# Optimization experiments

Hardware: AMD Instinct MI355X
Metric: run time of the kernel (lower is better)

Reference implementation:

```python
import jax, jax.numpy as jnp
import numpy as np

B, CF, HH, WW = 32, 768, 28, 28
M, NH = 32, 1024
BETA = 0.05

def _lin(key, out_d, in_d):
    k1, k2 = jax.random.split(key)
    s = 1.0 / np.sqrt(in_d)
    W = jax.random.uniform(k1, (out_d, in_d), minval=-s, maxval=s, dtype=jnp.float32)
    b = jax.random.uniform(k2, (out_d,), minval=-s, maxval=s, dtype=jnp.float32)
    return W, b

def setup_inputs() -> dict:
    key = jax.random.key(0)
    ks = jax.random.split(key, 16)
    inp = {
        'F': jax.random.normal(ks[0], (B, CF, HH, WW), dtype=jnp.float32),
        'A': jax.random.uniform(ks[1], (B, M, HH, WW), dtype=jnp.float32),
        'C': jax.random.normal(ks[2], (1, M * CF), dtype=jnp.float32),
    }
    names = ['xi', 'hi', 'xf', 'hf', 'xo', 'ho', 'xc', 'hc']
    for i, n in enumerate(names):
        in_d = CF if n[0] == 'x' else NH
        W, b = _lin(ks[3 + i], NH, in_d)
        inp['W' + n] = W
        inp['b' + n] = b
    return inp

def reference(F, A, C, Wxi, bxi, Whi, bhi, Wxf, bxf, Whf, bhf, Wxo, bxo, Who, bho, Wxc, bxc, Whc, bhc):
    b = F.shape[0]
    hw = F.shape[2] * F.shape[3]
    m = A.shape[1]
    # BAP: avg-pool of F * A_i over spatial dims, for each attention map -> [B, M, Cf]
    V = jnp.einsum('bchw,bmhw->bmc', F, A) / hw
    V = V.reshape(b, -1)  # [B, M*Cf]
    # RCLoss (center update + detached MSE)
    tmp = jnp.sum(V - C, axis=0)  # [M*Cf]
    C_new = C + (BETA * tmp / b)[None, :]
    diff = jax.lax.stop_gradient(V) - jax.lax.stop_gradient(C_new)
    rcloss = jnp.mean(diff * diff)
    # LSTM over M steps (note: original uses sigmoid for all gates via Sig_i)
    X_seq = V.reshape(b, m, -1).transpose(1, 0, 2)  # [M, B, Cf]
    h0 = jnp.zeros((b, Whi.shape[0]), dtype=V.dtype)
    c0 = jnp.zeros((b, Whi.shape[0]), dtype=V.dtype)
    def step(carry, X):
        H, Cc = carry
        I = jax.nn.sigmoid(X @ Wxi.T + bxi + H @ Whi.T + bhi)
        Fg = jax.nn.sigmoid(X @ Wxf.T + bxf + H @ Whf.T + bhf)
        O = jax.nn.sigmoid(X @ Wxo.T + bxo + H @ Who.T + bho)
        Ct = jnp.tanh(X @ Wxc.T + bxc + H @ Whc.T + bhc)
        Cc = Fg * Cc + I * Ct
        H = O * jnp.tanh(Cc)
        return (H, Cc), None
    (H, _), _ = jax.lax.scan(step, (h0, c0), X_seq)
    return (H, rcloss, C_new)
```

## Files before the change

kernel.cpp:

```cpp
#include <hip/hip_runtime.h>
#include <math.h>

#define CF 768
#define MM 32
#define HW 784
#define MCF 24576
#define BETA 0.05f

typedef __attribute__((ext_vector_type(8))) short bf16x8;
typedef __attribute__((ext_vector_type(4))) float f32x4;

__device__ __forceinline__ unsigned short bf16rne(float x) {
    unsigned int bits = __float_as_uint(x);
    unsigned int r = (bits + 0x7fffu + ((bits >> 16) & 1u)) >> 16;
    return (unsigned short)r;
}
__device__ __forceinline__ float bf2f(unsigned short u) {
    return __uint_as_float(((unsigned int)u) << 16);
}
__device__ __forceinline__ float sigf(float x) { return 1.f / (1.f + __expf(-x)); }
__device__ __forceinline__ float ftanh(float x) {
    x = fminf(fmaxf(x, -12.f), 12.f);
    float e = __expf(2.f * x);
    return (e - 1.f) / (e + 1.f);
}

__device__ __forceinline__ void cvt8(const float4 a, const float4 b, unsigned short* u) {
    u[0] = bf16rne(a.x); u[1] = bf16rne(a.y); u[2] = bf16rne(a.z); u[3] = bf16rne(a.w);
    u[4] = bf16rne(b.x); u[5] = bf16rne(b.y); u[6] = bf16rne(b.z); u[7] = bf16rne(b.w);
}

__global__ __launch_bounds__(256) void kA3(const float* __restrict__ F,
                                           const float* __restrict__ Ain,
                                           unsigned short* __restrict__ Vbf) {
    __shared__ unsigned short Alds[3328 * 8];
    __shared__ unsigned short Flds[2][512 * 8];
    const int bid = blockIdx.x;
    const int b = bid / 12, ct = bid - b * 12;
    const int cbase = ct * 64;
    const int t = threadIdx.x;
    const int lane = t & 63, w = t >> 6;
    const int n = lane & 15, q = lane >> 4;

    {
        float4 va[7][2];
        #pragma unroll
        for (int it = 0; it < 7; ++it) {
            int s = it * 256 + t;
            int lf = s & 63, mk = s >> 6;
            int m = (mk & 1) * 16 + (lf & 15);
            int k = (mk >> 1) * 32 + (lf >> 4) * 8;
            if (k < 784) {
                const float* src = Ain + ((size_t)(b * 32 + m)) * 784 + k;
                va[it][0] = *(const float4*)src;
                va[it][1] = *(const float4*)(src + 4);
            } else {
                va[it][0] = (float4){0, 0, 0, 0};
                va[it][1] = (float4){0, 0, 0, 0};
            }
        }
        #pragma unroll
        for (int it = 0; it < 7; ++it) {
            int s = it * 256 + t;
            unsigned short u[8];
            cvt8(va[it][0], va[it][1], u);
            *(uint4*)&Alds[s * 8] = *(const uint4*)u;
        }
        float4 vb[6][2];
        #pragma unroll
        for (int it = 0; it < 6; ++it) {
            int s = (it + 7) * 256 + t;
            int lf = s & 63, mk = s >> 6;
            int m = (mk & 1) * 16 + (lf & 15);
            int k = (mk >> 1) * 32 + (lf >> 4) * 8;
            if (k < 784) {
                const float* src = Ain + ((size_t)(b * 32 + m)) * 784 + k;
                vb[it][0] = *(const float4*)src;
                vb[it][1] = *(const float4*)(src + 4);
            } else {
                vb[it][0] = (float4){0, 0, 0, 0};
                vb[it][1] = (float4){0, 0, 0, 0};
            }
        }
        #pragma unroll
        for (int it = 0; it < 6; ++it) {
            int s = (it + 7) * 256 + t;
            unsigned short u[8];
            cvt8(vb[it][0], vb[it][1], u);
            *(uint4*)&Alds[s * 8] = *(const uint4*)u;
        }
    }

    float4 pf[2][2];
    const int s0 = t, s1 = t + 256;
    const int ls0 = s0 & 63, kc20 = (s0 >> 6) & 1, nt0 = s0 >> 7;
    const int ls1 = s1 & 63, kc21 = (s1 >> 6) & 1, nt1 = s1 >> 7;
    const int fc0 = nt0 * 16 + (ls0 & 15), fk0 = kc20 * 32 + (ls0 >> 4) * 8;
    const int fc1 = nt1 * 16 + (ls1 & 15), fk1 = kc21 * 32 + (ls1 >> 4) * 8;
    const float* Fr0 = F + ((size_t)(b * 768) + cbase + fc0) * 784;
    const float* Fr1 = F + ((size_t)(b * 768) + cbase + fc1) * 784;
    pf[0][0] = *(const float4*)(Fr0 + fk0); pf[0][1] = *(const float4*)(Fr0 + fk0 + 4);
    pf[1][0] = *(const float4*)(Fr1 + fk1); pf[1][1] = *(const float4*)(Fr1 + fk1 + 4);
    {
        unsigned short u[8];
        cvt8(pf[0][0], pf[0][1], u); *(uint4*)&Flds[0][s0 * 8] = *(const uint4*)u;
        cvt8(pf[1][0], pf[1][1], u); *(uint4*)&Flds[0][s1 * 8] = *(const uint4*)u;
    }
    __syncthreads();

    f32x4 acc[2];
    acc[0] = (f32x4){0, 0, 0, 0};
    acc[1] = (f32x4){0, 0, 0, 0};

    for (int c13 = 0; c13 < 13; ++c13) {
        const int buf = c13 & 1;
        if (c13 < 12) {
            int k0 = (c13 + 1) * 64 + fk0;
            int k1 = (c13 + 1) * 64 + fk1;
            if (k0 < 784) {
                pf[0][0] = *(const float4*)(Fr0 + k0); pf[0][1] = *(const float4*)(Fr0 + k0 + 4);
            } else { pf[0][0] = (float4){0,0,0,0}; pf[0][1] = (float4){0,0,0,0}; }
            if (k1 < 784) {
                pf[1][0] = *(const float4*)(Fr1 + k1); pf[1][1] = *(const float4*)(Fr1 + k1 + 4);
            } else { pf[1][0] = (float4){0,0,0,0}; pf[1][1] = (float4){0,0,0,0}; }
        }
        #pragma unroll
        for (int kc2 = 0; kc2 < 2; ++kc2) {
            const int kc = c13 * 2 + kc2;
            bf16x8 bfr = *(const bf16x8*)&Flds[buf][((w * 2 + kc2) * 64 + lane) * 8];
            bf16x8 a0 = *(const bf16x8*)&Alds[((kc * 2 + 0) * 64 + lane) * 8];
            bf16x8 a1 = *(const bf16x8*)&Alds[((kc * 2 + 1) * 64 + lane) * 8];
            acc[0] = __builtin_amdgcn_mfma_f32_16x16x32_bf16(a0, bfr, acc[0], 0, 0, 0);
            acc[1] = __builtin_amdgcn_mfma_f32_16x16x32_bf16(a1, bfr, acc[1], 0, 0, 0);
        }
        if (c13 < 12) {
            unsigned short u[8];
            cvt8(pf[0][0], pf[0][1], u); *(uint4*)&Flds[buf ^ 1][s0 * 8] = *(const uint4*)u;
            cvt8(pf[1][0], pf[1][1], u); *(uint4*)&Flds[buf ^ 1][s1 * 8] = *(const uint4*)u;
        }
        __syncthreads();
    }

    #pragma unroll
    for (int mt = 0; mt < 2; ++mt)
        #pragma unroll
        for (int r = 0; r < 4; ++r)
            Vbf[(size_t)(b * 32 + mt * 16 + q * 4 + r) * 768 + cbase + w * 16 + n] =
                bf16rne(acc[mt][r] * (1.f / 784.f));
}

__global__ __launch_bounds__(256) void kMisc(
    const unsigned short* __restrict__ Vbf, const float* __restrict__ C,
    float* __restrict__ Cnew_out, float* __restrict__ partial,
    const float* __restrict__ Wxi, const float* __restrict__ Wxf,
    const float* __restrict__ Wxo, const float* __restrict__ Wxc,
    unsigned short* __restrict__ Wxbf,
    const float* __restrict__ Whi, const float* __restrict__ Whf,
    const float* __restrict__ Who, const float* __restrict__ Whc,
    unsigned short* __restrict__ Wbf) {
    const int bid = blockIdx.x;
    if (bid < 96) {
        int j = bid * 256 + threadIdx.x;
        float c = C[j];
        float s = 0.f;
        for (int b = 0; b < 32; ++b) s += bf2f(Vbf[(size_t)b * MCF + j]);
        float cn = c + BETA * (s * (1.f / 32.f) - c);
        Cnew_out[j] = cn;
        float ds = 0.f;
        for (int b = 0; b < 32; ++b) {
            float d = bf2f(Vbf[(size_t)b * MCF + j]) - cn;
            ds = fmaf(d, d, ds);
        }
        __shared__ float red[256];
        red[threadIdx.x] = ds;
        __syncthreads();
        for (int off = 128; off > 0; off >>= 1) {
            if (threadIdx.x < off) red[threadIdx.x] += red[threadIdx.x + off];
            __syncthreads();
        }
        if (threadIdx.x == 0) partial[bid] = red[0];
    } else if (bid < 1632) {
        int gid = (bid - 96) * 256 + threadIdx.x;
        int row = gid / 96;
        int kq = (gid - row * 96) * 8;
        int g = row >> 10, j = row & 1023;
        const float* Wg = (g == 0) ? Wxi : (g == 1) ? Wxf : (g == 2) ? Wxo : Wxc;
        const float* src = Wg + (size_t)j * CF + kq;
        float4 f0 = *(const float4*)src;
        float4 f1 = *(const float4*)(src + 4);
        unsigned short u[8];
        cvt8(f0, f1, u);
        *(uint4*)&Wxbf[(size_t)row * CF + kq] = *(const uint4*)u;
    } else {
        size_t tid8 = ((size_t)(bid - 1632) * 256 + threadIdx.x) * 8;
        int row = (int)(tid8 >> 10);
        int k = (int)(tid8 & 1023);
        int g = row >> 10, j = row & 1023;
        const float* Wg = (g == 0) ? Whi : (g == 1) ? Whf : (g == 2) ? Who : Whc;
        const float* src = Wg + (size_t)j * 1024 + k;
        float4 f0 = *(const float4*)src;
        float4 f1 = *(const float4*)(src + 4);
        unsigned short u[8];
        cvt8(f0, f1, u);
        *(uint4*)&Wbf[tid8] = *(const uint4*)u;
    }
}

__global__ __launch_bounds__(512) void kC3(
    const unsigned short* __restrict__ Vbf,
    const unsigned short* __restrict__ Wxbf,
    const float* __restrict__ bxi, const float* __restrict__ bxf,
    const float* __restrict__ bxo, const float* __restrict__ bxc,
    const float* __restrict__ bhi, const float* __restrict__ bhf,
    const float* __restrict__ bho, const float* __restrict__ bhc,
    unsigned short* __restrict__ Xbf,
    const float* __restrict__ partial, float* __restrict__ outRC) {
    __shared__ unsigned short Asg[512 * 8];
    const int bx = blockIdx.x;
    const int by = blockIdx.y;
    const int t = threadIdx.x;
    const int lane = t & 63;
    const int w = t >> 6;
    const int n = lane & 15;
    const int q = lane >> 4;
    const int mbase = bx * 64;

    const int st_row = (w & 3) * 16 + n;
    const int st_kb  = (w >> 2) * 4 + q;
    const int st_rg  = mbase + st_row;
    const int st_vrow = (st_rg & 31) * 32 + (st_rg >> 5);
    const unsigned short* st_src = Vbf + (size_t)st_vrow * CF + st_kb * 8;

    const int nb = by * 128 + w * 16;
    const unsigned short* Brow = Wxbf + (size_t)(nb + n) * CF + q * 8;

    f32x4 acc[4];
    #pragma unroll
    for (int g = 0; g < 4; ++g) acc[g] = (f32x4){0.f, 0.f, 0.f, 0.f};

    uint4 st = *(const uint4*)st_src;
    for (int kc = 0; kc < 12; ++kc) {
        __syncthreads();
        *(uint4*)&Asg[t * 8] = st;
        __syncthreads();
        if (kc + 1 < 12) st = *(const uint4*)(st_src + (kc + 1) * 64);
        #pragma unroll
        for (int p = 0; p < 2; ++p) {
            bf16x8 bfr = *(const bf16x8*)(Brow + kc * 64 + p * 32);
            #pragma unroll
            for (int g = 0; g < 4; ++g) {
                bf16x8 a = *(const bf16x8*)&Asg[((p * 4 + g) * 64 + lane) * 8];
                acc[g] = __builtin_amdgcn_mfma_f32_16x16x32_bf16(a, bfr, acc[g], 0, 0, 0);
            }
        }
    }

    const int gg = by >> 3;
    const int j = (by & 7) * 128 + w * 16 + n;
    const float* bx_ = (gg == 0) ? bxi : (gg == 1) ? bxf : (gg == 2) ? bxo : bxc;
    const float* bh_ = (gg == 0) ? bhi : (gg == 1) ? bhf : (gg == 2) ? bho : bhc;
    const float bias = bx_[j] + bh_[j];
    #pragma unroll
    for (int g = 0; g < 4; ++g) {
        #pragma unroll
        for (int rr = 0; rr < 4; ++rr) {
            int rg = mbase + g * 16 + q * 4 + rr;
            int tt = rg >> 5, bb = rg & 31;
            Xbf[((size_t)(tt * 4 + gg) * 32 + bb) * 1024 + j] = bf16rne(acc[g][rr] + bias);
        }
    }

    if (bx == 0 && by == 31) {
        __syncthreads();
        float* red = (float*)Asg;
        float v = (t < 96) ? partial[t] : 0.f;
        red[t] = v;
        __syncthreads();
        for (int off = 256; off > 0; off >>= 1) {
            if (t < off) red[t] += red[t + off];
            __syncthreads();
        }
        if (t == 0) outRC[0] = red[0] / (32.f * 24576.f);
    }
}

__global__ __launch_bounds__(512) void kStep(
    const unsigned short* __restrict__ Wbf,
    const unsigned short* __restrict__ Xbf,
    const unsigned short* __restrict__ Hprev,
    unsigned short* __restrict__ Hnext,
    float* __restrict__ Cst,
    float* __restrict__ outH,
    int step) {
    __shared__ float pbuf[8][32][17];
    __shared__ float sbuf[32][17];
    const int bi = blockIdx.x;
    const int jbase = bi * 4;
    const int t = threadIdx.x;
    const int lane = t & 63;
    const int w = t >> 6;
    const int n = lane & 15;
    const int q = lane >> 4;

    const int pb = t >> 4, pnn = t & 15;
    const int pg = pnn >> 2, pjj = pnn & 3;
    const float xv = bf2f(Xbf[(((size_t)step * 4 + pg) * 32 + pb) * 1024 + jbase + pjj]);
    float cprev = 0.f;
    if (step > 0 && t < 128) cprev = Cst[(t >> 2) * 1024 + jbase + (t & 3)];

    if (step > 0) {
        const int g = n >> 2, jj = n & 3;
        const unsigned short* Wrow = Wbf + ((size_t)(g * 1024 + jbase + jj)) * 1024 + w * 128;
        const unsigned short* hb0 = Hprev + (size_t)n * 1024 + w * 128;
        const unsigned short* hb1 = Hprev + (size_t)(n + 16) * 1024 + w * 128;
        f32x4 acc0 = {0.f, 0.f, 0.f, 0.f};
        f32x4 acc1 = {0.f, 0.f, 0.f, 0.f};
        #pragma unroll
        for (int ks = 0; ks < 4; ++ks) {
            int k = ks * 32 + q * 8;
            bf16x8 bfrag = *(const bf16x8*)(Wrow + k);
            bf16x8 a0 = *(const bf16x8*)(hb0 + k);
            bf16x8 a1 = *(const bf16x8*)(hb1 + k);
            acc0 = __builtin_amdgcn_mfma_f32_16x16x32_bf16(a0, bfrag, acc0, 0, 0, 0);
            acc1 = __builtin_amdgcn_mfma_f32_16x16x32_bf16(a1, bfrag, acc1, 0, 0, 0);
        }
        #pragma unroll
        for (int r = 0; r < 4; ++r) {
            pbuf[w][q * 4 + r][n] = acc0[r];
            pbuf[w][16 + q * 4 + r][n] = acc1[r];
        }
    }
    __syncthreads();
    {
        float s = xv;
        if (step > 0) {
            #pragma unroll
            for (int w2 = 0; w2 < 8; ++w2) s += pbuf[w2][pb][pnn];
        }
        sbuf[pb][pnn] = s;
    }
    __syncthreads();
    if (t < 128) {
        int b = t >> 2, jj = t & 3;
        float I  = sigf(sbuf[b][jj]);
        float Fg = sigf(sbuf[b][4 + jj]);
        float O  = sigf(sbuf[b][8 + jj]);
        float Ct = ftanh(sbuf[b][12 + jj]);
        float c = fmaf(Fg, cprev, I * Ct);
        Cst[b * 1024 + jbase + jj] = c;
        float h = O * ftanh(c);
        if (step < 31) {
            Hnext[b * 1024 + jbase + jj] = bf16rne(h);
        } else {
            outH[b * 1024 + jbase + jj] = h;
        }
    }
}

extern "C" void kernel_launch(void* const* d_in, const int* in_sizes, int n_in,
                              void* d_out, int out_size, void* d_ws, size_t ws_size,
                              hipStream_t stream) {
    const float* F   = (const float*)d_in[0];
    const float* A   = (const float*)d_in[1];
    const float* C   = (const float*)d_in[2];
    const float* Wxi = (const float*)d_in[3];
    const float* bxi = (const float*)d_in[4];
    const float* Whi = (const float*)d_in[5];
    const float* bhi = (const float*)d_in[6];
    const float* Wxf = (const float*)d_in[7];
    const float* bxf = (const float*)d_in[8];
    const float* Whf = (const float*)d_in[9];
    const float* bhf = (const float*)d_in[10];
    const float* Wxo = (const float*)d_in[11];
    const float* bxo = (const float*)d_in[12];
    const float* Who = (const float*)d_in[13];
    const float* bho = (const float*)d_in[14];
    const float* Wxc = (const float*)d_in[15];
    const float* bxc = (const float*)d_in[16];
    const float* Whc = (const float*)d_in[17];
    const float* bhc = (const float*)d_in[18];

    float* out   = (float*)d_out;
    float* outH  = out;
    float* outRC = out + 32768;
    float* outC  = out + 32769;

    float* ws = (float*)d_ws;
    unsigned short* Xbf  = (unsigned short*)ws;
    unsigned short* Wxbf = (unsigned short*)(ws + 2097152);
    unsigned short* Wbf  = (unsigned short*)(ws + 3670016);
    unsigned short* Vbf  = (unsigned short*)(ws + 5767168);
    float* part = ws + 6160384;
    unsigned short* Hbf = (unsigned short*)(ws + 6160480);
    float* Cst  = ws + 6193248;

    kA3<<<dim3(384), 256, 0, stream>>>(F, A, Vbf);
    kMisc<<<dim3(3680), 256, 0, stream>>>(Vbf, C, outC, part,
                                          Wxi, Wxf, Wxo, Wxc, Wxbf,
                                          Whi, Whf, Who, Whc, Wbf);
    kC3<<<dim3(16, 32), 512, 0, stream>>>(Vbf, Wxbf,
                                          bxi, bxf, bxo, bxc,
                                          bhi, bhf, bho, bhc, Xbf,
                                          part, outRC);

    for (int step = 0; step < 32; ++step) {
        const unsigned short* Hprev = Hbf + ((step + 1) & 1) * 32768;
        unsigned short* Hnext = (unsigned short*)(Hbf + (step & 1) * 32768);
        kStep<<<dim3(256), 512, 0, stream>>>(Wbf, Xbf, Hprev, Hnext, Cst, outH, step);
    }
}
```

Before: 228.3 us.

## Fuse 32 LSTM step launches into one persistent kernel with atomic step barriers

Replaces the per-timestep kernel loop with a single persistent kernel of 128 blocks. Each block owns 8 hidden units, keeps the cell state in registers, and waits on per-step atomic counters (grouped by block index mod 8) before reading the previous hidden state. The previous hidden state is staged in shared memory per half of K, and the new hidden state is written to a rotating per-step buffer. This removes 31 kernel-launch boundaries and the global cell-state round trip, at the cost of spin-waiting and relying on all 128 blocks being co-resident.

```diff
diff --git a/kernel.cpp b/kernel.cpp
--- a/kernel.cpp
+++ b/kernel.cpp
@@ -284,75 +284,121 @@
     }
 }
 
-__global__ __launch_bounds__(512) void kStep(
+__global__ __launch_bounds__(1024) void kLP(
     const unsigned short* __restrict__ Wbf,
     const unsigned short* __restrict__ Xbf,
-    const unsigned short* __restrict__ Hprev,
-    unsigned short* __restrict__ Hnext,
-    float* __restrict__ Cst,
-    float* __restrict__ outH,
-    int step) {
-    __shared__ float pbuf[8][32][17];
-    __shared__ float sbuf[32][17];
+    unsigned short* __restrict__ Hrot,
+    unsigned int* __restrict__ cnt,
+    float* __restrict__ outH) {
+    __shared__ char smem[65536];
+    unsigned short* Hs = (unsigned short*)smem;
+    float* pb = (float*)(smem + 32768);
+    float* sb = (float*)smem;
     const int bi = blockIdx.x;
-    const int jbase = bi * 4;
+    const int jbase = bi * 8;
     const int t = threadIdx.x;
     const int lane = t & 63;
     const int w = t >> 6;
-    const int n = lane & 15;
-    const int q = lane >> 4;
-
-    const int pb = t >> 4, pnn = t & 15;
-    const int pg = pnn >> 2, pjj = pnn & 3;
-    const float xv = bf2f(Xbf[(((size_t)step * 4 + pg) * 32 + pb) * 1024 + jbase + pjj]);
-    float cprev = 0.f;
-    if (step > 0 && t < 128) cprev = Cst[(t >> 2) * 1024 + jbase + (t & 3)];
-
-    if (step > 0) {
-        const int g = n >> 2, jj = n & 3;
-        const unsigned short* Wrow = Wbf + ((size_t)(g * 1024 + jbase + jj)) * 1024 + w * 128;
-        const unsigned short* hb0 = Hprev + (size_t)n * 1024 + w * 128;
-        const unsigned short* hb1 = Hprev + (size_t)(n + 16) * 1024 + w * 128;
+    const int nh = w & 1, kw = w >> 1;
+    const int n16 = lane & 15, q = lane >> 4;
+
+    const int rown = nh * 16 + n16;
+    const int gB = rown >> 3, jjB = rown & 7;
+    const unsigned short* Wrow = Wbf + ((size_t)(gB * 1024 + jbase + jjB)) * 1024;
+
+    const int cb = t >> 2, cjp = t & 3;
+    float creg0 = 0.f, creg1 = 0.f;
+
+    for (int step = 0; step < 32; ++step) {
+        unsigned int xv0 = 0, xv1 = 0, xv2 = 0, xv3 = 0;
+        if (t < 128) {
+            xv0 = *(const unsigned int*)&Xbf[(((size_t)step * 4 + 0) * 32 + cb) * 1024 + jbase + cjp * 2];
+            xv1 = *(const unsigned int*)&Xbf[(((size_t)step * 4 + 1) * 32 + cb) * 1024 + jbase + cjp * 2];
+            xv2 = *(const unsigned int*)&Xbf[(((size_t)step * 4 + 2) * 32 + cb) * 1024 + jbase + cjp * 2];
+            xv3 = *(const unsigned int*)&Xbf[(((size_t)step * 4 + 3) * 32 + cb) * 1024 + jbase + cjp * 2];
+        }
+        if (step > 0 && t < 8) {
+            while (atomicAdd(&cnt[(step - 1) * 8 + t], 0u) < 16u)
+                __builtin_amdgcn_s_sleep(8);
+        }
+        __syncthreads();
+
         f32x4 acc0 = {0.f, 0.f, 0.f, 0.f};
         f32x4 acc1 = {0.f, 0.f, 0.f, 0.f};
-        #pragma unroll
-        for (int ks = 0; ks < 4; ++ks) {
-            int k = ks * 32 + q * 8;
-            bf16x8 bfrag = *(const bf16x8*)(Wrow + k);
-            bf16x8 a0 = *(const bf16x8*)(hb0 + k);
-            bf16x8 a1 = *(const bf16x8*)(hb1 + k);
-            acc0 = __builtin_amdgcn_mfma_f32_16x16x32_bf16(a0, bfrag, acc0, 0, 0, 0);
-            acc1 = __builtin_amdgcn_mfma_f32_16x16x32_bf16(a1, bfrag, acc1, 0, 0, 0);
-        }
-        #pragma unroll
-        for (int r = 0; r < 4; ++r) {
-            pbuf[w][q * 4 + r][n] = acc0[r];
-            pbuf[w][16 + q * 4 + r][n] = acc1[r];
-        }
-    }
-    __syncthreads();
-    {
-        float s = xv;
         if (step > 0) {
+            const unsigned short* Hprev = Hrot + (size_t)(step - 1) * 32768;
             #pragma unroll
-            for (int w2 = 0; w2 < 8; ++w2) s += pbuf[w2][pb][pnn];
-        }
-        sbuf[pb][pnn] = s;
-    }
-    __syncthreads();
-    if (t < 128) {
-        int b = t >> 2, jj = t & 3;
-        float I  = sigf(sbuf[b][jj]);
-        float Fg = sigf(sbuf[b][4 + jj]);
-        float O  = sigf(sbuf[b][8 + jj]);
-        float Ct = ftanh(sbuf[b][12 + jj]);
-        float c = fmaf(Fg, cprev, I * Ct);
-        Cst[b * 1024 + jbase + jj] = c;
-        float h = O * ftanh(c);
+            for (int half = 0; half < 2; ++half) {
+                #pragma unroll
+                for (int ss = 0; ss < 2; ++ss) {
+                    int s = t + ss * 1024;
+                    int ls = s & 63, grp = s >> 6;
+                    int mt_ = grp & 1, kc_ = grp >> 1;
+                    int m = mt_ * 16 + (ls & 15);
+                    int kk = kc_ * 32 + (ls >> 4) * 8;
+                    uint4 d = *(const uint4*)(Hprev + (size_t)m * 1024 + half * 512 + kk);
+                    *(uint4*)&Hs[(size_t)s * 8] = d;
+                }
+                __syncthreads();
+                #pragma unroll
+                for (int kc2 = 0; kc2 < 2; ++kc2) {
+                    int kcl = kw * 2 + kc2;
+                    bf16x8 bfr = *(const bf16x8*)(Wrow + half * 512 + kcl * 32 + q * 8);
+                    bf16x8 a0 = *(const bf16x8*)&Hs[((kcl * 2 + 0) * 64 + lane) * 8];
+                    bf16x8 a1 = *(const bf16x8*)&Hs[((kcl * 2 + 1) * 64 + lane) * 8];
+                    acc0 = __builtin_amdgcn_mfma_f32_16x16x32_bf16(a0, bfr, acc0, 0, 0, 0);
+                    acc1 = __builtin_amdgcn_mfma_f32_16x16x32_bf16(a1, bfr, acc1, 0, 0, 0);
+                }
+                __syncthreads();
+            }
+            #pragma unroll
+            for (int r = 0; r < 4; ++r) {
+                pb[((kw * 2 + nh) * 2 + 0) * 256 + (q * 4 + r) * 16 + n16] = acc0[r];
+                pb[((kw * 2 + nh) * 2 + 1) * 256 + (q * 4 + r) * 16 + n16] = acc1[r];
+            }
+        }
+        __syncthreads();
+        {
+            int b = t >> 5, r = t & 31;
+            float s = 0.f;
+            if (step > 0) {
+                int mt_ = b >> 4, m16 = b & 15, nh_ = r >> 4, nn = r & 15;
+                #pragma unroll
+                for (int k8 = 0; k8 < 8; ++k8)
+                    s += pb[((k8 * 2 + nh_) * 2 + mt_) * 256 + m16 * 16 + nn];
+            }
+            sb[r * 33 + b] = s;
+        }
+        __syncthreads();
+        if (t < 128) {
+            float p0 = bf2f((unsigned short)(xv0 & 0xffff)) + sb[(0 * 8 + cjp * 2) * 33 + cb];
+            float p1 = bf2f((unsigned short)(xv1 & 0xffff)) + sb[(1 * 8 + cjp * 2) * 33 + cb];
+            float p2 = bf2f((unsigned short)(xv2 & 0xffff)) + sb[(2 * 8 + cjp * 2) * 33 + cb];
+            float p3 = bf2f((unsigned short)(xv3 & 0xffff)) + sb[(3 * 8 + cjp * 2) * 33 + cb];
+            float I0 = sigf(p0), F0 = sigf(p1), O0 = sigf(p2), T0 = ftanh(p3);
+            creg0 = fmaf(F0, creg0, I0 * T0);
+            float h0 = O0 * ftanh(creg0);
+            float q0 = bf2f((unsigned short)(xv0 >> 16)) + sb[(0 * 8 + cjp * 2 + 1) * 33 + cb];
+            float q1 = bf2f((unsigned short)(xv1 >> 16)) + sb[(1 * 8 + cjp * 2 + 1) * 33 + cb];
+            float q2 = bf2f((unsigned short)(xv2 >> 16)) + sb[(2 * 8 + cjp * 2 + 1) * 33 + cb];
+            float q3 = bf2f((unsigned short)(xv3 >> 16)) + sb[(3 * 8 + cjp * 2 + 1) * 33 + cb];
+            float I1 = sigf(q0), F1 = sigf(q1), O1 = sigf(q2), T1 = ftanh(q3);
+            creg1 = fmaf(F1, creg1, I1 * T1);
+            float h1 = O1 * ftanh(creg1);
+
+            if (step < 31) {
+                unsigned int packed = (unsigned int)bf16rne(h0) | ((unsigned int)bf16rne(h1) << 16);
+                unsigned int* dst = (unsigned int*)(Hrot + (size_t)step * 32768);
+                atomicExch(dst + (cb * 512 + (jbase >> 1) + cjp), packed);
+            } else {
+                float2 hv; hv.x = h0; hv.y = h1;
+                *(float2*)&outH[cb * 1024 + jbase + cjp * 2] = hv;
+            }
+        }
         if (step < 31) {
-            Hnext[b * 1024 + jbase + jj] = bf16rne(h);
-        } else {
-            outH[b * 1024 + jbase + jj] = h;
+            asm volatile("s_waitcnt vmcnt(0)" ::: "memory");
+            __syncthreads();
+            if (t == 0) atomicAdd(&cnt[step * 8 + (bi & 7)], 1u);
         }
     }
 }
@@ -391,9 +437,10 @@
     unsigned short* Wbf  = (unsigned short*)(ws + 3670016);
     unsigned short* Vbf  = (unsigned short*)(ws + 5767168);
     float* part = ws + 6160384;
-    unsigned short* Hbf = (unsigned short*)(ws + 6160480);
-    float* Cst  = ws + 6193248;
-
+    unsigned short* Hrot = (unsigned short*)(ws + 6160480);
+    unsigned int* cnt = (unsigned int*)(ws + 6684768);
+
+    hipMemsetAsync(cnt, 0, 256 * sizeof(unsigned int), stream);
     kA3<<<dim3(384), 256, 0, stream>>>(F, A, Vbf);
     kMisc<<<dim3(3680), 256, 0, stream>>>(Vbf, C, outC, part,
                                           Wxi, Wxf, Wxo, Wxc, Wxbf,
@@ -402,10 +449,5 @@
                                           bxi, bxf, bxo, bxc,
                                           bhi, bhf, bho, bhc, Xbf,
                                           part, outRC);
-
-    for (int step = 0; step < 32; ++step) {
-        const unsigned short* Hprev = Hbf + ((step + 1) & 1) * 32768;
-        unsigned short* Hnext = (unsigned short*)(Hbf + (step & 1) * 32768);
-        kStep<<<dim3(256), 512, 0, stream>>>(Wbf, Xbf, Hprev, Hnext, Cst, outH, step);
-    }
-}
+    kLP<<<dim3(128), 1024, 0, stream>>>(Wbf, Xbf, Hrot, cnt, outH);
+}
```

New measurement: 278.7 us. 22.1% more time.

## Fold weight conversion into BAP kernel and RC-loss into input-GEMM kernel

Applied to the files above, without the earlier changes.

Removes the separate kMisc launch. The fp32→bf16 weight conversion blocks now run as extra blocks of the BAP kernel, so they overlap with the MFMA work. The center-update and RC-loss reduction run as extra blocks of the input-projection GEMM kernel and accumulate into the output with atomicAdd. This saves one launch and one serialization point. The cost is a float atomic accumulation order, which makes the loss sum order nondeterministic, and a mixed-workload grid in the first kernel.

```diff
diff --git a/kernel.cpp b/kernel.cpp
--- a/kernel.cpp
+++ b/kernel.cpp
@@ -30,15 +30,53 @@
     u[4] = bf16rne(b.x); u[5] = bf16rne(b.y); u[6] = bf16rne(b.z); u[7] = bf16rne(b.w);
 }
 
-__global__ __launch_bounds__(256) void kA3(const float* __restrict__ F,
-                                           const float* __restrict__ Ain,
-                                           unsigned short* __restrict__ Vbf) {
+__global__ __launch_bounds__(256) void kA3M(
+    const float* __restrict__ F, const float* __restrict__ Ain,
+    unsigned short* __restrict__ Vbf,
+    const float* __restrict__ Wxi, const float* __restrict__ Wxf,
+    const float* __restrict__ Wxo, const float* __restrict__ Wxc,
+    unsigned short* __restrict__ Wxbf,
+    const float* __restrict__ Whi, const float* __restrict__ Whf,
+    const float* __restrict__ Who, const float* __restrict__ Whc,
+    unsigned short* __restrict__ Wbf,
+    float* __restrict__ outRC) {
     __shared__ unsigned short Alds[3328 * 8];
     __shared__ unsigned short Flds[2][512 * 8];
     const int bid = blockIdx.x;
+    const int t = threadIdx.x;
+
+    if (bid >= 384) {
+        if (bid == 384 && t == 0) outRC[0] = 0.f;
+        if (bid < 1920) {
+            int gid = (bid - 384) * 256 + t;
+            int row = gid / 96;
+            int kq = (gid - row * 96) * 8;
+            int g = row >> 10, j = row & 1023;
+            const float* Wg = (g == 0) ? Wxi : (g == 1) ? Wxf : (g == 2) ? Wxo : Wxc;
+            const float* src = Wg + (size_t)j * CF + kq;
+            float4 f0 = *(const float4*)src;
+            float4 f1 = *(const float4*)(src + 4);
+            unsigned short u[8];
+            cvt8(f0, f1, u);
+            *(uint4*)&Wxbf[(size_t)row * CF + kq] = *(const uint4*)u;
+        } else {
+            size_t tid8 = ((size_t)(bid - 1920) * 256 + t) * 8;
+            int row = (int)(tid8 >> 10);
+            int k = (int)(tid8 & 1023);
+            int g = row >> 10, j = row & 1023;
+            const float* Wg = (g == 0) ? Whi : (g == 1) ? Whf : (g == 2) ? Who : Whc;
+            const float* src = Wg + (size_t)j * 1024 + k;
+            float4 f0 = *(const float4*)src;
+            float4 f1 = *(const float4*)(src + 4);
+            unsigned short u[8];
+            cvt8(f0, f1, u);
+            *(uint4*)&Wbf[tid8] = *(const uint4*)u;
+        }
+        return;
+    }
+
     const int b = bid / 12, ct = bid - b * 12;
     const int cbase = ct * 64;
-    const int t = threadIdx.x;
     const int lane = t & 63, w = t >> 6;
     const int n = lane & 15, q = lane >> 4;
 
@@ -149,64 +187,7 @@
                 bf16rne(acc[mt][r] * (1.f / 784.f));
 }
 
-__global__ __launch_bounds__(256) void kMisc(
-    const unsigned short* __restrict__ Vbf, const float* __restrict__ C,
-    float* __restrict__ Cnew_out, float* __restrict__ partial,
-    const float* __restrict__ Wxi, const float* __restrict__ Wxf,
-    const float* __restrict__ Wxo, const float* __restrict__ Wxc,
-    unsigned short* __restrict__ Wxbf,
-    const float* __restrict__ Whi, const float* __restrict__ Whf,
-    const float* __restrict__ Who, const float* __restrict__ Whc,
-    unsigned short* __restrict__ Wbf) {
-    const int bid = blockIdx.x;
-    if (bid < 96) {
-        int j = bid * 256 + threadIdx.x;
-        float c = C[j];
-        float s = 0.f;
-        for (int b = 0; b < 32; ++b) s += bf2f(Vbf[(size_t)b * MCF + j]);
-        float cn = c + BETA * (s * (1.f / 32.f) - c);
-        Cnew_out[j] = cn;
-        float ds = 0.f;
-        for (int b = 0; b < 32; ++b) {
-            float d = bf2f(Vbf[(size_t)b * MCF + j]) - cn;
-            ds = fmaf(d, d, ds);
-        }
-        __shared__ float red[256];
-        red[threadIdx.x] = ds;
-        __syncthreads();
-        for (int off = 128; off > 0; off >>= 1) {
-            if (threadIdx.x < off) red[threadIdx.x] += red[threadIdx.x + off];
-            __syncthreads();
-        }
-        if (threadIdx.x == 0) partial[bid] = red[0];
-    } else if (bid < 1632) {
-        int gid = (bid - 96) * 256 + threadIdx.x;
-        int row = gid / 96;
-        int kq = (gid - row * 96) * 8;
-        int g = row >> 10, j = row & 1023;
-        const float* Wg = (g == 0) ? Wxi : (g == 1) ? Wxf : (g == 2) ? Wxo : Wxc;
-        const float* src = Wg + (size_t)j * CF + kq;
-        float4 f0 = *(const float4*)src;
-        float4 f1 = *(const float4*)(src + 4);
-        unsigned short u[8];
-        cvt8(f0, f1, u);
-        *(uint4*)&Wxbf[(size_t)row * CF + kq] = *(const uint4*)u;
-    } else {
-        size_t tid8 = ((size_t)(bid - 1632) * 256 + threadIdx.x) * 8;
-        int row = (int)(tid8 >> 10);
-        int k = (int)(tid8 & 1023);
-        int g = row >> 10, j = row & 1023;
-        const float* Wg = (g == 0) ? Whi : (g == 1) ? Whf : (g == 2) ? Who : Whc;
-        const float* src = Wg + (size_t)j * 1024 + k;
-        float4 f0 = *(const float4*)src;
-        float4 f1 = *(const float4*)(src + 4);
-        unsigned short u[8];
-        cvt8(f0, f1, u);
-        *(uint4*)&Wbf[tid8] = *(const uint4*)u;
-    }
-}
-
-__global__ __launch_bounds__(512) void kC3(
+__global__ __launch_bounds__(512) void kC3B(
     const unsigned short* __restrict__ Vbf,
     const unsigned short* __restrict__ Wxbf,
     const float* __restrict__ bxi, const float* __restrict__ bxf,
@@ -214,11 +195,41 @@
     const float* __restrict__ bhi, const float* __restrict__ bhf,
     const float* __restrict__ bho, const float* __restrict__ bhc,
     unsigned short* __restrict__ Xbf,
-    const float* __restrict__ partial, float* __restrict__ outRC) {
+    const float* __restrict__ C, float* __restrict__ Cnew_out,
+    float* __restrict__ outRC) {
     __shared__ unsigned short Asg[512 * 8];
     const int bx = blockIdx.x;
     const int by = blockIdx.y;
     const int t = threadIdx.x;
+
+    if (bx >= 16) {
+        int e = (bx - 16) * 32 + by;
+        if (e < 48) {
+            int j = e * 512 + t;
+            float c = C[j];
+            float s = 0.f;
+            #pragma unroll 4
+            for (int b = 0; b < 32; ++b) s += bf2f(Vbf[(size_t)b * MCF + j]);
+            float cn = c + BETA * (s * (1.f / 32.f) - c);
+            Cnew_out[j] = cn;
+            float ds = 0.f;
+            #pragma unroll 4
+            for (int b = 0; b < 32; ++b) {
+                float d = bf2f(Vbf[(size_t)b * MCF + j]) - cn;
+                ds = fmaf(d, d, ds);
+            }
+            float* red = (float*)Asg;
+            red[t] = ds;
+            __syncthreads();
+            for (int off = 256; off > 0; off >>= 1) {
+                if (t < off) red[t] += red[t + off];
+                __syncthreads();
+            }
+            if (t == 0) atomicAdd(outRC, red[0] * (1.f / (32.f * 24576.f)));
+        }
+        return;
+    }
+
     const int lane = t & 63;
     const int w = t >> 6;
     const int n = lane & 15;
@@ -268,19 +279,6 @@
             int tt = rg >> 5, bb = rg & 31;
             Xbf[((size_t)(tt * 4 + gg) * 32 + bb) * 1024 + j] = bf16rne(acc[g][rr] + bias);
         }
-    }
-
-    if (bx == 0 && by == 31) {
-        __syncthreads();
-        float* red = (float*)Asg;
-        float v = (t < 96) ? partial[t] : 0.f;
-        red[t] = v;
-        __syncthreads();
-        for (int off = 256; off > 0; off >>= 1) {
-            if (t < off) red[t] += red[t + off];
-            __syncthreads();
-        }
-        if (t == 0) outRC[0] = red[0] / (32.f * 24576.f);
     }
 }
 
@@ -390,18 +388,16 @@
     unsigned short* Wxbf = (unsigned short*)(ws + 2097152);
     unsigned short* Wbf  = (unsigned short*)(ws + 3670016);
     unsigned short* Vbf  = (unsigned short*)(ws + 5767168);
-    float* part = ws + 6160384;
-    unsigned short* Hbf = (unsigned short*)(ws + 6160480);
-    float* Cst  = ws + 6193248;
-
-    kA3<<<dim3(384), 256, 0, stream>>>(F, A, Vbf);
-    kMisc<<<dim3(3680), 256, 0, stream>>>(Vbf, C, outC, part,
-                                          Wxi, Wxf, Wxo, Wxc, Wxbf,
-                                          Whi, Whf, Who, Whc, Wbf);
-    kC3<<<dim3(16, 32), 512, 0, stream>>>(Vbf, Wxbf,
-                                          bxi, bxf, bxo, bxc,
-                                          bhi, bhf, bho, bhc, Xbf,
-                                          part, outRC);
+    unsigned short* Hbf  = (unsigned short*)(ws + 6160384);
+    float* Cst  = ws + 6193152;
+
+    kA3M<<<dim3(3968), 256, 0, stream>>>(F, A, Vbf,
+                                         Wxi, Wxf, Wxo, Wxc, Wxbf,
+                                         Whi, Whf, Who, Whc, Wbf, outRC);
+    kC3B<<<dim3(18, 32), 512, 0, stream>>>(Vbf, Wxbf,
+                                           bxi, bxf, bxo, bxc,
+                                           bhi, bhf, bho, bhc, Xbf,
+                                           C, outC, outRC);
 
     for (int step = 0; step < 32; ++step) {
         const unsigned short* Hprev = Hbf + ((step + 1) & 1) * 32768;
```

After: 234.4 us. +2.7%, slower.
